# Kernel tuning notes

Measured on AMD Instinct MI355X. Metric: run time of the kernel, lower is better.

The kernel has to match this reference:

```python
import jax, jax.numpy as jnp
import numpy as np
import math

D_MODEL = 128
N_HEADS = 8
D_FF = 512
FACTOR = 3
EPS = 1e-5


def _ln(x, g, b):
    mu = x.mean(-1, keepdims=True)
    var = ((x - mu) ** 2).mean(-1, keepdims=True)
    return (x - mu) / jnp.sqrt(var + EPS) * g + b


def setup_inputs() -> dict:
    key = jax.random.key(0)
    ks = jax.random.split(key, 16)
    d, dff = D_MODEL, D_FF
    s = 0.02
    return {
        "x": jax.random.normal(ks[0], (4, 32, 256), dtype=jnp.float32),
        "mlp_w": jax.random.normal(ks[1], (d,)) * s,  # Conv2d(1,d,1x1) weight squeezed
        "mlp_b": jnp.zeros((d,), jnp.float32),
        "wq": jax.random.normal(ks[2], (d, d)) * s, "bq": jnp.zeros((d,), jnp.float32),
        "wk": jax.random.normal(ks[3], (d, d)) * s, "bk": jnp.zeros((d,), jnp.float32),
        "wv": jax.random.normal(ks[4], (d, d)) * s, "bv": jnp.zeros((d,), jnp.float32),
        "wo": jax.random.normal(ks[5], (d, d)) * s, "bo": jnp.zeros((d,), jnp.float32),
        "w1": jax.random.normal(ks[6], (dff, d)) * s, "b1": jnp.zeros((dff,), jnp.float32),
        "w2": jax.random.normal(ks[7], (d, dff)) * s, "b2": jnp.zeros((d,), jnp.float32),
        "ln1_g": jnp.ones((d,), jnp.float32), "ln1_b": jnp.zeros((d,), jnp.float32),
        "ln2_g": jnp.ones((d,), jnp.float32), "ln2_b": jnp.zeros((d,), jnp.float32),
    }


def reference(x, mlp_w, mlp_b, wq, bq, wk, bk, wv, bv, wo, bo,
              w1, b1, w2, b2, ln1_g, ln1_b, ln2_g, ln2_b):
    b, N, T = x.shape
    C, H = D_MODEL, N_HEADS
    E = C // H
    # 1x1 Conv2d from 1 channel -> per-channel affine of scalar input
    h = x[..., None] * mlp_w + mlp_b                      # [b,N,T,C]
    h = h.reshape(b * N, T, C)                            # [B,L,C]
    B, L = h.shape[0], T
    q = (h @ wq.T + bq).reshape(B, L, H, E).transpose(0, 2, 1, 3)  # [B,H,L,E]
    k = (h @ wk.T + bk).reshape(B, L, H, E).transpose(0, 2, 1, 3)
    v = (h @ wv.T + bv).reshape(B, L, H, E).transpose(0, 2, 1, 3)

    sample_k = min(FACTOR * math.ceil(math.log(L)), L)
    u = min(FACTOR * math.ceil(math.log(L)), L)
    # random K-sample indices shared across batch/heads (torch.randint analogue)
    idx = jax.random.randint(jax.random.key(42), (L, sample_k), 0, L)

    scores_full = jnp.einsum('bhle,bhse->bhls', q, k)     # [B,H,L,L]
    qk_sample = jnp.take_along_axis(scores_full, idx[None, None], axis=-1)  # [B,H,L,sample_k]
    M = qk_sample.max(-1) - qk_sample.sum(-1) / L         # sparsity measure
    m_top = jax.lax.top_k(M, u)[1]                        # [B,H,u] top-u query indices
    scores_top = jnp.take_along_axis(scores_full, m_top[..., None], axis=2)  # [B,H,u,L]
    scores_top = scores_top / math.sqrt(E)

    attn = jax.nn.softmax(scores_top, axis=-1)
    upd = jnp.einsum('bhul,bhle->bhue', attn, v)          # [B,H,u,E]
    # mask_flag=False: initial context = mean(V) broadcast over queries
    context = jnp.broadcast_to(v.mean(axis=2, keepdims=True), v.shape)
    bi = jnp.arange(B)[:, None, None]
    hi = jnp.arange(H)[None, :, None]
    context = context.at[bi, hi, m_top].set(upd)          # scatter top-u updates

    out = context.transpose(0, 2, 1, 3).reshape(B, L, C) @ wo.T + bo
    x1 = _ln(h + out, ln1_g, ln1_b)
    y = jax.nn.relu(x1 @ w1.T + b1) @ w2.T + b2           # 1x1 conv1d pair == MLP
    out2 = _ln(x1 + y, ln2_g, ln2_b)
    out2 = out2.reshape(b, N, T, C).sum(axis=1)           # sum over N
    return out2.transpose(0, 2, 1)                        # [b,C,T]
```

## Files before the change

kernel.cpp:

```cpp
#include <hip/hip_runtime.h>
#include <stdint.h>
#include <math.h>


#define EPSF 1e-5f

typedef short bf16x8 __attribute__((ext_vector_type(8)));
typedef float f32x4  __attribute__((ext_vector_type(4)));

__device__ __forceinline__ unsigned short f2bf(float f) {
  union { float f; unsigned u; } v; v.f = f;
  unsigned r = v.u + 0x7FFFu + ((v.u >> 16) & 1u);
  return (unsigned short)(r >> 16);
}
__device__ __forceinline__ float bf2f(unsigned short u) {
  union { unsigned u; float f; } v; v.u = ((unsigned)u) << 16;
  return v.f;
}
__device__ __forceinline__ float waveSum(float v) {
  #pragma unroll
  for (int m = 32; m > 0; m >>= 1) v += __shfl_xor(v, m);
  return v;
}

__device__ __forceinline__ void threefry2x32_k42(uint32_t& x0, uint32_t& x1) {
  const uint32_t ks0 = 0u, ks1 = 42u, ks2 = 0u ^ 42u ^ 0x1BD11BDAu;
  x0 += ks0; x1 += ks1;
#define TF_R(d) { x0 += x1; x1 = (x1 << d) | (x1 >> (32 - d)); x1 ^= x0; }
  TF_R(13) TF_R(15) TF_R(26) TF_R(6)  x0 += ks1; x1 += ks2 + 1u;
  TF_R(17) TF_R(29) TF_R(16) TF_R(24) x0 += ks2; x1 += ks0 + 2u;
  TF_R(13) TF_R(15) TF_R(26) TF_R(6)  x0 += ks0; x1 += ks1 + 3u;
  TF_R(17) TF_R(29) TF_R(16) TF_R(24) x0 += ks1; x1 += ks2 + 4u;
  TF_R(13) TF_R(15) TF_R(26) TF_R(6)  x0 += ks2; x1 += ks0 + 5u;
#undef TF_R
}

__global__ __launch_bounds__(256) void setup_kernel(
    const float* __restrict__ mlp_w, const float* __restrict__ mlp_b,
    const float* __restrict__ wq, const float* __restrict__ bq,
    const float* __restrict__ wk, const float* __restrict__ bk,
    const float* __restrict__ wv, const float* __restrict__ bv,
    const float* __restrict__ wo, const float* __restrict__ bo,
    const float* __restrict__ w1, const float* __restrict__ w2,
    int* __restrict__ idxT, float* __restrict__ cst,
    unsigned short* __restrict__ w1bf, unsigned short* __restrict__ w2bf) {
  int tid = threadIdx.x;
  {
    int gid = blockIdx.x * 256 + tid;
    int base = gid * 16;
    const float* src; unsigned short* dst; int off;
    if (base < 65536) { src = w1; dst = w1bf; off = base; }
    else              { src = w2; dst = w2bf; off = base - 65536; }
    #pragma unroll 4
    for (int k = 0; k < 16; k++) dst[off + k] = f2bf(src[off + k]);
  }
  if (blockIdx.x != 0) return;
  for (int p = tid; p < 2304; p += 256) {
    uint32_t a = (uint32_t)p, bb = (uint32_t)(p + 2304);
    threefry2x32_k42(a, bb);
    int l0 = p / 18, j0 = p - l0 * 18;
    int p2 = p + 2304;
    int l1 = p2 / 18, j1 = p2 - l1 * 18;
    idxT[j0 * 256 + l0] = (int)(a & 0xFFu);
    idxT[j1 * 256 + l1] = (int)(bb & 0xFFu);
  }
  if (tid < 128) {
    float aq = 0.f, cq_ = 0.f, ak = 0.f, ck_ = 0.f, av = 0.f, cv_ = 0.f;
    for (int c = 0; c < 128; c++) {
      float w = mlp_w[c], bb = mlp_b[c];
      float q = wq[tid * 128 + c], k = wk[tid * 128 + c], v = wv[tid * 128 + c];
      aq += q * w; cq_ += q * bb;
      ak += k * w; ck_ += k * bb;
      av += v * w; cv_ += v * bb;
    }
    cst[0   + tid] = aq;
    cst[128 + tid] = cq_ + bq[tid];
    cst[256 + tid] = ak;
    cst[384 + tid] = ck_ + bk[tid];
    cst[512 + tid] = av;
    cst[640 + tid] = cv_ + bv[tid];
  }
  __syncthreads();
  if (tid < 8) {
    float a = 0.f, b = 0.f, g = 0.f, d = 0.f;
    for (int e = 0; e < 16; e++) {
      int j = tid * 16 + e;
      float Aq = cst[j], Cq = cst[128 + j], Ak = cst[256 + j], Ck = cst[384 + j];
      a += Aq * Ak; b += Aq * Ck; g += Cq * Ak; d += Cq * Ck;
    }
    cst[768 + tid] = a; cst[776 + tid] = b; cst[784 + tid] = g; cst[792 + tid] = d;
  }
  if (tid < 128) {
    float oc = 0.f;
    for (int h = 0; h < 8; h++) {
      float s = 0.f;
      for (int e = 0; e < 16; e++) {
        float w = wo[tid * 128 + h * 16 + e];
        s  += w * cst[512 + h * 16 + e];
        oc += w * cst[640 + h * 16 + e];
      }
      cst[800 + h * 128 + tid] = s;
    }
    cst[1824 + tid] = oc + bo[tid] + mlp_b[tid];
  }
}

__global__ __launch_bounds__(256) void attn_kernel(
    const float* __restrict__ x, const int* __restrict__ idxT,
    const float* __restrict__ cst, float* __restrict__ g) {
  __shared__ float xr[256];
  __shared__ float Mb[512];
  __shared__ float selv[512];
  __shared__ float rsum[4], rmax[4], rmin[4];
  __shared__ int   items[64];
  __shared__ float witem[64];
  __shared__ int   cnt;
  int tid = threadIdx.x, lane = tid & 63, w = tid >> 6;
  int seq = blockIdx.x >> 2, hg = blockIdx.x & 3;
  if (tid == 0) cnt = 0;
  float xv = x[seq * 256 + tid];
  xr[tid] = xv;
  float s = waveSum(xv);
  float mx = xv, mn = xv;
  #pragma unroll
  for (int m = 32; m > 0; m >>= 1) {
    mx = fmaxf(mx, __shfl_xor(mx, m));
    mn = fminf(mn, __shfl_xor(mn, m));
  }
  if (lane == 0) { rsum[w] = s; rmax[w] = mx; rmin[w] = mn; }
  __syncthreads();
  float meanx = (rsum[0] + rsum[1] + rsum[2] + rsum[3]) * (1.0f / 256.0f);
  float maxx = fmaxf(fmaxf(rmax[0], rmax[1]), fmaxf(rmax[2], rmax[3]));
  float minx = fminf(fminf(rmin[0], rmin[1]), fminf(rmin[2], rmin[3]));
  int l32 = tid & 31, grp = tid >> 5;
  float xs8[8];
  #pragma unroll
  for (int k = 0; k < 8; k++) xs8[k] = xr[l32 + k * 32];
  float mx18 = -INFINITY, mn18 = INFINITY, s18 = 0.f;
  #pragma unroll 3
  for (int j = 0; j < 18; j++) {
    float xs = xr[idxT[j * 256 + tid]];
    mx18 = fmaxf(mx18, xs); mn18 = fminf(mn18, xs); s18 += xs;
  }
  int h0 = hg * 2, h1 = h0 + 1;
  float al0 = cst[768 + h0], be0 = cst[776 + h0], ga0 = cst[784 + h0], de0 = cst[792 + h0];
  float al1 = cst[768 + h1], be1 = cst[776 + h1], ga1 = cst[784 + h1], de1 = cst[792 + h1];
  float ac0 = fmaf(al0, xv, ga0), cc0 = fmaf(be0, xv, de0);
  float ac1 = fmaf(al1, xv, ga1), cc1 = fmaf(be1, xv, de1);
  float M0 = ((ac0 >= 0.f ? ac0 * mx18 : ac0 * mn18) + cc0)
           - (fmaf(ac0, s18, 18.f * cc0)) * (1.0f / 256.0f);
  float M1 = ((ac1 >= 0.f ? ac1 * mx18 : ac1 * mn18) + cc1)
           - (fmaf(ac1, s18, 18.f * cc1)) * (1.0f / 256.0f);
  Mb[tid] = M0; Mb[256 + tid] = M1;
  __syncthreads();
  int r0 = 0, r1 = 0;
  const float4* Mb4 = (const float4*)Mb;
  #pragma unroll 4
  for (int j4 = 0; j4 < 64; j4++) {
    float4 a = Mb4[j4], bb = Mb4[64 + j4];
    int base = j4 * 4;
    r0 += (a.x > M0) || (a.x == M0 && base     < tid);
    r0 += (a.y > M0) || (a.y == M0 && base + 1 < tid);
    r0 += (a.z > M0) || (a.z == M0 && base + 2 < tid);
    r0 += (a.w > M0) || (a.w == M0 && base + 3 < tid);
    r1 += (bb.x > M1) || (bb.x == M1 && base     < tid);
    r1 += (bb.y > M1) || (bb.y == M1 && base + 1 < tid);
    r1 += (bb.z > M1) || (bb.z == M1 && base + 2 < tid);
    r1 += (bb.w > M1) || (bb.w == M1 && base + 3 < tid);
  }
  selv[tid] = meanx; selv[256 + tid] = meanx;
  if (r0 < 18) { int p = atomicAdd(&cnt, 1); items[p] = tid;       witem[p] = 0.25f * ac0; }
  if (r1 < 18) { int p = atomicAdd(&cnt, 1); items[p] = 256 + tid; witem[p] = 0.25f * ac1; }
  __syncthreads();
  int nIt = cnt;
  for (int i = grp; i < nIt; i += 8) {
    int it = items[i]; float wv = witem[i];
    float m0 = (wv >= 0.f) ? wv * maxx : wv * minx;
    float S1 = 0.f, Sx = 0.f;
    #pragma unroll
    for (int k = 0; k < 8; k++) {
      float e = __expf(fmaf(wv, xs8[k], -m0));
      S1 += e; Sx = fmaf(xs8[k], e, Sx);
    }
    #pragma unroll
    for (int m = 16; m > 0; m >>= 1) {
      S1 += __shfl_xor(S1, m); Sx += __shfl_xor(Sx, m);
    }
    if (l32 == 0) selv[it] = Sx / S1;
  }
  __syncthreads();
  float2 gv; gv.x = selv[tid]; gv.y = selv[256 + tid];
  *(float2*)&g[(size_t)((seq << 8) + tid) * 8 + hg * 2] = gv;
}

__global__ __launch_bounds__(256, 4) void mega_kernel(
    const float* __restrict__ x, const float* __restrict__ g,
    const float* __restrict__ cst, const float* __restrict__ mlp_w,
    const unsigned short* __restrict__ w1bf, const float* __restrict__ b1,
    const unsigned short* __restrict__ w2bf, const float* __restrict__ b2,
    const float* __restrict__ ln1g, const float* __restrict__ ln1b,
    const float* __restrict__ ln2g, const float* __restrict__ ln2b,
    float* __restrict__ out) {
  __shared__ unsigned short x1s[32 * 136];
  __shared__ char ovl[32 * 264 * 2];
  __shared__ float psum[512];
  unsigned short* a1s = (unsigned short*)ovl;
  float*          zbuf = (float*)ovl;
  int tid = threadIdx.x, lane = tid & 63, w = tid >> 6;
  int col = lane & 15, quad = lane >> 4;
  int b = blockIdx.x >> 8, t = blockIdx.x & 255;

  {
    int c0 = lane << 1;
    float mwa = mlp_w[c0], mwb = mlp_w[c0 | 1];
    float cca = cst[1824 + c0], ccb = cst[1824 + (c0 | 1)];
    float wva[8], wvb[8];
    #pragma unroll
    for (int h = 0; h < 8; h++) {
      wva[h] = cst[800 + h * 128 + c0];
      wvb[h] = cst[800 + h * 128 + (c0 | 1)];
    }
    float g1a = ln1g[c0], g1b = ln1g[c0 | 1];
    float e1a = ln1b[c0], e1b = ln1b[c0 | 1];
    for (int tk = 0; tk < 8; tk++) {
      int n = w * 8 + tk;
      int tok = ((b * 32 + n) << 8) + t;
      float xvv = x[tok];
      float4 gA = *(const float4*)(g + (size_t)tok * 8);
      float4 gB = *(const float4*)(g + (size_t)tok * 8 + 4);
      float ra = fmaf(xvv, mwa, cca), rb = fmaf(xvv, mwb, ccb);
      ra = fmaf(gA.x, wva[0], ra); rb = fmaf(gA.x, wvb[0], rb);
      ra = fmaf(gA.y, wva[1], ra); rb = fmaf(gA.y, wvb[1], rb);
      ra = fmaf(gA.z, wva[2], ra); rb = fmaf(gA.z, wvb[2], rb);
      ra = fmaf(gA.w, wva[3], ra); rb = fmaf(gA.w, wvb[3], rb);
      ra = fmaf(gB.x, wva[4], ra); rb = fmaf(gB.x, wvb[4], rb);
      ra = fmaf(gB.y, wva[5], ra); rb = fmaf(gB.y, wvb[5], rb);
      ra = fmaf(gB.z, wva[6], ra); rb = fmaf(gB.z, wvb[6], rb);
      ra = fmaf(gB.w, wva[7], ra); rb = fmaf(gB.w, wvb[7], rb);
      float su = waveSum(ra + rb);
      float mu = su * (1.0f / 128.0f);
      float da = ra - mu, db = rb - mu;
      float vs = waveSum(da * da + db * db);
      float inv = rsqrtf(vs * (1.0f / 128.0f) + EPSF);
      unsigned int pa = f2bf(da * inv * g1a + e1a);
      unsigned int pb = f2bf(db * inv * g1b + e1b);
      *(unsigned int*)&x1s[n * 136 + c0] = pa | (pb << 16);
    }
  }
  __syncthreads();

  f32x4 acc2[4];
  #pragma unroll
  for (int i = 0; i < 4; i++) acc2[i] = (f32x4){0.f, 0.f, 0.f, 0.f};

  for (int fh = 0; fh < 2; fh++) {
    f32x4 acc1[8];
    #pragma unroll
    for (int i = 0; i < 8; i++) acc1[i] = (f32x4){0.f, 0.f, 0.f, 0.f};
    #pragma unroll
    for (int ks = 0; ks < 4; ks++) {
      bf16x8 af[2];
      #pragma unroll
      for (int rg = 0; rg < 2; rg++)
        af[rg] = *(const bf16x8*)&x1s[(rg * 16 + col) * 136 + ks * 32 + quad * 8];
      #pragma unroll
      for (int ft = 0; ft < 4; ft++) {
        int f = fh * 256 + w * 64 + ft * 16 + col;
        bf16x8 bfr = *(const bf16x8*)(w1bf + f * 128 + ks * 32 + quad * 8);
        #pragma unroll
        for (int rg = 0; rg < 2; rg++)
          acc1[rg * 4 + ft] = __builtin_amdgcn_mfma_f32_16x16x32_bf16(
              af[rg], bfr, acc1[rg * 4 + ft], 0, 0, 0);
      }
    }
    if (fh) __syncthreads();
    #pragma unroll
    for (int ft = 0; ft < 4; ft++) {
      int fl = w * 64 + ft * 16 + col;
      float bv = b1[fh * 256 + fl];
      #pragma unroll
      for (int rg = 0; rg < 2; rg++) {
        f32x4 a = acc1[rg * 4 + ft];
        #pragma unroll
        for (int r = 0; r < 4; r++) {
          float vv = fmaxf(a[r] + bv, 0.f);
          a1s[(rg * 16 + quad * 4 + r) * 264 + fl] = f2bf(vv);
        }
      }
    }
    __syncthreads();
    #pragma unroll
    for (int ks = 0; ks < 8; ks++) {
      bf16x8 a2[2];
      #pragma unroll
      for (int rg = 0; rg < 2; rg++)
        a2[rg] = *(const bf16x8*)&a1s[(rg * 16 + col) * 264 + ks * 32 + quad * 8];
      #pragma unroll
      for (int tc = 0; tc < 2; tc++) {
        int c = w * 32 + tc * 16 + col;
        bf16x8 bfr = *(const bf16x8*)(w2bf + c * 512 + fh * 256 + ks * 32 + quad * 8);
        #pragma unroll
        for (int rg = 0; rg < 2; rg++)
          acc2[rg * 2 + tc] = __builtin_amdgcn_mfma_f32_16x16x32_bf16(
              a2[rg], bfr, acc2[rg * 2 + tc], 0, 0, 0);
      }
    }
  }
  __syncthreads();

  #pragma unroll
  for (int tc = 0; tc < 2; tc++) {
    int c = w * 32 + tc * 16 + col;
    float b2c = b2[c];
    #pragma unroll
    for (int rg = 0; rg < 2; rg++) {
      #pragma unroll
      for (int r = 0; r < 4; r++) {
        int row = rg * 16 + quad * 4 + r;
        float z = acc2[rg * 2 + tc][r] + b2c + bf2f(x1s[row * 136 + c]);
        zbuf[row * 132 + c] = z;
      }
    }
  }
  __syncthreads();

  {
    int rloc = lane & 7, part = lane >> 3;
    int row = w * 8 + rloc;
    float4 zv[4];
    #pragma unroll
    for (int q = 0; q < 4; q++)
      zv[q] = *(const float4*)&zbuf[row * 132 + part * 16 + q * 4];
    float s = 0.f;
    #pragma unroll
    for (int q = 0; q < 4; q++) s += zv[q].x + zv[q].y + zv[q].z + zv[q].w;
    s += __shfl_xor(s, 8); s += __shfl_xor(s, 16); s += __shfl_xor(s, 32);
    float mu = s * (1.0f / 128.0f);
    float ss = 0.f;
    #pragma unroll
    for (int q = 0; q < 4; q++) {
      float d0 = zv[q].x - mu, d1 = zv[q].y - mu, d2 = zv[q].z - mu, d3 = zv[q].w - mu;
      ss += d0 * d0 + d1 * d1 + d2 * d2 + d3 * d3;
    }
    ss += __shfl_xor(ss, 8); ss += __shfl_xor(ss, 16); ss += __shfl_xor(ss, 32);
    float inv = rsqrtf(ss * (1.0f / 128.0f) + EPSF);
    float4 o[4];
    #pragma unroll
    for (int q = 0; q < 4; q++) {
      float4 g2v = *(const float4*)(ln2g + part * 16 + q * 4);
      float4 e2v = *(const float4*)(ln2b + part * 16 + q * 4);
      o[q].x = (zv[q].x - mu) * inv * g2v.x + e2v.x;
      o[q].y = (zv[q].y - mu) * inv * g2v.y + e2v.y;
      o[q].z = (zv[q].z - mu) * inv * g2v.z + e2v.z;
      o[q].w = (zv[q].w - mu) * inv * g2v.w + e2v.w;
    }
    #pragma unroll
    for (int m = 1; m <= 4; m <<= 1) {
      #pragma unroll
      for (int q = 0; q < 4; q++) {
        o[q].x += __shfl_xor(o[q].x, m);
        o[q].y += __shfl_xor(o[q].y, m);
        o[q].z += __shfl_xor(o[q].z, m);
        o[q].w += __shfl_xor(o[q].w, m);
      }
    }
    if (rloc == 0) {
      #pragma unroll
      for (int q = 0; q < 4; q++)
        *(float4*)&psum[w * 128 + part * 16 + q * 4] = o[q];
    }
  }
  __syncthreads();
  if (tid < 128) {
    int c = tid;
    float v = psum[c] + psum[128 + c] + psum[256 + c] + psum[384 + c];
    out[(size_t)(b * 128 + c) * 256 + t] = v;
  }
}

extern "C" void kernel_launch(void* const* d_in, const int* in_sizes, int n_in,
                              void* d_out, int out_size, void* d_ws, size_t ws_size,
                              hipStream_t stream) {
  (void)in_sizes; (void)n_in; (void)out_size; (void)ws_size;
  const float* x    = (const float*)d_in[0];
  const float* mlpw = (const float*)d_in[1];
  const float* mlpb = (const float*)d_in[2];
  const float* wq   = (const float*)d_in[3];
  const float* bq   = (const float*)d_in[4];
  const float* wk   = (const float*)d_in[5];
  const float* bk   = (const float*)d_in[6];
  const float* wv   = (const float*)d_in[7];
  const float* bv   = (const float*)d_in[8];
  const float* wo   = (const float*)d_in[9];
  const float* bo   = (const float*)d_in[10];
  const float* w1   = (const float*)d_in[11];
  const float* b1   = (const float*)d_in[12];
  const float* w2   = (const float*)d_in[13];
  const float* b2   = (const float*)d_in[14];
  const float* ln1g = (const float*)d_in[15];
  const float* ln1b = (const float*)d_in[16];
  const float* ln2g = (const float*)d_in[17];
  const float* ln2b = (const float*)d_in[18];

  char* ws = (char*)d_ws;
  int*            idxT = (int*)(ws);
  float*          cst  = (float*)(ws + 20480);
  unsigned short* w1bf = (unsigned short*)(ws + 32768);
  unsigned short* w2bf = (unsigned short*)(ws + 163840);
  float*          gbuf = (float*)(ws + 294912);
  float*          outp = (float*)d_out;

  hipLaunchKernelGGL(setup_kernel, dim3(32), dim3(256), 0, stream,
                     mlpw, mlpb, wq, bq, wk, bk, wv, bv, wo, bo, w1, w2,
                     idxT, cst, w1bf, w2bf);
  hipLaunchKernelGGL(attn_kernel, dim3(512), dim3(256), 0, stream,
                     x, idxT, cst, gbuf);
  hipLaunchKernelGGL(mega_kernel, dim3(1024), dim3(256), 0, stream,
                     x, gbuf, cst, mlpw, w1bf, b1, w2bf, b2,
                     ln1g, ln1b, ln2g, ln2b, outp);
}
```

Measured before the change: 163.7 us.

## Split FFN by hidden chunks per wave, removing block barriers between GEMMs

Restructures the MLP in the fused kernel so each wave owns a 128-wide slice of the hidden dimension. It computes its partial FFN2 output over all 128 channels using a private LDS tile, so the barriers between FFN1 and FFN2 are no longer needed. The partial sums from the four waves are reduced through LDS in bf16 before LayerNorm2, which adds precision loss and extra LDS traffic. It also batches four tokens in the LN1 prologue to overlap the shuffle reductions, and lowers the launch-bounds occupancy hint from 4 to 3 to leave room for the larger accumulator set.

```diff
diff --git a/kernel.cpp b/kernel.cpp
--- a/kernel.cpp
+++ b/kernel.cpp
@@ -193,7 +193,7 @@
   *(float2*)&g[(size_t)((seq << 8) + tid) * 8 + hg * 2] = gv;
 }
 
-__global__ __launch_bounds__(256, 4) void mega_kernel(
+__global__ __launch_bounds__(256, 3) void mega_kernel(
     const float* __restrict__ x, const float* __restrict__ g,
     const float* __restrict__ cst, const float* __restrict__ mlp_w,
     const unsigned short* __restrict__ w1bf, const float* __restrict__ b1,
@@ -202,13 +202,12 @@
     const float* __restrict__ ln2g, const float* __restrict__ ln2b,
     float* __restrict__ out) {
   __shared__ unsigned short x1s[32 * 136];
-  __shared__ char ovl[32 * 264 * 2];
+  __shared__ unsigned short tbuf[4 * 2304];
   __shared__ float psum[512];
-  unsigned short* a1s = (unsigned short*)ovl;
-  float*          zbuf = (float*)ovl;
   int tid = threadIdx.x, lane = tid & 63, w = tid >> 6;
   int col = lane & 15, quad = lane >> 4;
   int b = blockIdx.x >> 8, t = blockIdx.x & 255;
+  unsigned short* tb = tbuf + w * 2304;
 
   {
     int c0 = lane << 1;
@@ -222,159 +221,194 @@
     }
     float g1a = ln1g[c0], g1b = ln1g[c0 | 1];
     float e1a = ln1b[c0], e1b = ln1b[c0 | 1];
-    for (int tk = 0; tk < 8; tk++) {
-      int n = w * 8 + tk;
-      int tok = ((b * 32 + n) << 8) + t;
-      float xvv = x[tok];
-      float4 gA = *(const float4*)(g + (size_t)tok * 8);
-      float4 gB = *(const float4*)(g + (size_t)tok * 8 + 4);
-      float ra = fmaf(xvv, mwa, cca), rb = fmaf(xvv, mwb, ccb);
-      ra = fmaf(gA.x, wva[0], ra); rb = fmaf(gA.x, wvb[0], rb);
-      ra = fmaf(gA.y, wva[1], ra); rb = fmaf(gA.y, wvb[1], rb);
-      ra = fmaf(gA.z, wva[2], ra); rb = fmaf(gA.z, wvb[2], rb);
-      ra = fmaf(gA.w, wva[3], ra); rb = fmaf(gA.w, wvb[3], rb);
-      ra = fmaf(gB.x, wva[4], ra); rb = fmaf(gB.x, wvb[4], rb);
-      ra = fmaf(gB.y, wva[5], ra); rb = fmaf(gB.y, wvb[5], rb);
-      ra = fmaf(gB.z, wva[6], ra); rb = fmaf(gB.z, wvb[6], rb);
-      ra = fmaf(gB.w, wva[7], ra); rb = fmaf(gB.w, wvb[7], rb);
-      float su = waveSum(ra + rb);
-      float mu = su * (1.0f / 128.0f);
-      float da = ra - mu, db = rb - mu;
-      float vs = waveSum(da * da + db * db);
-      float inv = rsqrtf(vs * (1.0f / 128.0f) + EPSF);
-      unsigned int pa = f2bf(da * inv * g1a + e1a);
-      unsigned int pb = f2bf(db * inv * g1b + e1b);
-      *(unsigned int*)&x1s[n * 136 + c0] = pa | (pb << 16);
-    }
-  }
-  __syncthreads();
-
-  f32x4 acc2[4];
-  #pragma unroll
-  for (int i = 0; i < 4; i++) acc2[i] = (f32x4){0.f, 0.f, 0.f, 0.f};
-
-  for (int fh = 0; fh < 2; fh++) {
-    f32x4 acc1[8];
-    #pragma unroll
-    for (int i = 0; i < 8; i++) acc1[i] = (f32x4){0.f, 0.f, 0.f, 0.f};
+    #pragma unroll
+    for (int bt = 0; bt < 2; bt++) {
+      float xv4[4]; float4 gA[4], gB[4];
+      #pragma unroll
+      for (int k = 0; k < 4; k++) {
+        int n = w * 8 + bt * 4 + k;
+        int tok = ((b * 32 + n) << 8) + t;
+        xv4[k] = x[tok];
+        gA[k] = *(const float4*)(g + (size_t)tok * 8);
+        gB[k] = *(const float4*)(g + (size_t)tok * 8 + 4);
+      }
+      float ra[4], rb[4], su[4];
+      #pragma unroll
+      for (int k = 0; k < 4; k++) {
+        float a_ = fmaf(xv4[k], mwa, cca), b_ = fmaf(xv4[k], mwb, ccb);
+        a_ = fmaf(gA[k].x, wva[0], a_); b_ = fmaf(gA[k].x, wvb[0], b_);
+        a_ = fmaf(gA[k].y, wva[1], a_); b_ = fmaf(gA[k].y, wvb[1], b_);
+        a_ = fmaf(gA[k].z, wva[2], a_); b_ = fmaf(gA[k].z, wvb[2], b_);
+        a_ = fmaf(gA[k].w, wva[3], a_); b_ = fmaf(gA[k].w, wvb[3], b_);
+        a_ = fmaf(gB[k].x, wva[4], a_); b_ = fmaf(gB[k].x, wvb[4], b_);
+        a_ = fmaf(gB[k].y, wva[5], a_); b_ = fmaf(gB[k].y, wvb[5], b_);
+        a_ = fmaf(gB[k].z, wva[6], a_); b_ = fmaf(gB[k].z, wvb[6], b_);
+        a_ = fmaf(gB[k].w, wva[7], a_); b_ = fmaf(gB[k].w, wvb[7], b_);
+        ra[k] = a_; rb[k] = b_; su[k] = a_ + b_;
+      }
+      #pragma unroll
+      for (int m = 32; m > 0; m >>= 1) {
+        su[0] += __shfl_xor(su[0], m); su[1] += __shfl_xor(su[1], m);
+        su[2] += __shfl_xor(su[2], m); su[3] += __shfl_xor(su[3], m);
+      }
+      float vs[4], da[4], db[4];
+      #pragma unroll
+      for (int k = 0; k < 4; k++) {
+        float mu = su[k] * (1.0f / 128.0f);
+        da[k] = ra[k] - mu; db[k] = rb[k] - mu;
+        vs[k] = da[k] * da[k] + db[k] * db[k];
+      }
+      #pragma unroll
+      for (int m = 32; m > 0; m >>= 1) {
+        vs[0] += __shfl_xor(vs[0], m); vs[1] += __shfl_xor(vs[1], m);
+        vs[2] += __shfl_xor(vs[2], m); vs[3] += __shfl_xor(vs[3], m);
+      }
+      #pragma unroll
+      for (int k = 0; k < 4; k++) {
+        int n = w * 8 + bt * 4 + k;
+        float inv = rsqrtf(vs[k] * (1.0f / 128.0f) + EPSF);
+        unsigned int pa = f2bf(da[k] * inv * g1a + e1a);
+        unsigned int pb = f2bf(db[k] * inv * g1b + e1b);
+        *(unsigned int*)&x1s[n * 136 + c0] = pa | (pb << 16);
+      }
+    }
+  }
+  __syncthreads();
+
+  float b1v[2][4];
+  #pragma unroll
+  for (int ch = 0; ch < 2; ch++)
+    #pragma unroll
+    for (int ft = 0; ft < 4; ft++)
+      b1v[ch][ft] = b1[w * 128 + ch * 64 + ft * 16 + col];
+
+  f32x4 acc2[2][8];
+  #pragma unroll
+  for (int i = 0; i < 2; i++)
+    #pragma unroll
+    for (int j = 0; j < 8; j++) acc2[i][j] = (f32x4){0.f, 0.f, 0.f, 0.f};
+
+  #pragma unroll
+  for (int ch = 0; ch < 2; ch++) {
+    int fbase = w * 128 + ch * 64;
+    f32x4 acc1[2][4];
+    #pragma unroll
+    for (int i = 0; i < 2; i++)
+      #pragma unroll
+      for (int j = 0; j < 4; j++) acc1[i][j] = (f32x4){0.f, 0.f, 0.f, 0.f};
     #pragma unroll
     for (int ks = 0; ks < 4; ks++) {
-      bf16x8 af[2];
-      #pragma unroll
-      for (int rg = 0; rg < 2; rg++)
-        af[rg] = *(const bf16x8*)&x1s[(rg * 16 + col) * 136 + ks * 32 + quad * 8];
+      bf16x8 a0 = *(const bf16x8*)&x1s[col * 136 + ks * 32 + quad * 8];
+      bf16x8 a1 = *(const bf16x8*)&x1s[(16 + col) * 136 + ks * 32 + quad * 8];
       #pragma unroll
       for (int ft = 0; ft < 4; ft++) {
-        int f = fh * 256 + w * 64 + ft * 16 + col;
-        bf16x8 bfr = *(const bf16x8*)(w1bf + f * 128 + ks * 32 + quad * 8);
-        #pragma unroll
-        for (int rg = 0; rg < 2; rg++)
-          acc1[rg * 4 + ft] = __builtin_amdgcn_mfma_f32_16x16x32_bf16(
-              af[rg], bfr, acc1[rg * 4 + ft], 0, 0, 0);
-      }
-    }
-    if (fh) __syncthreads();
+        int f = fbase + ft * 16 + col;
+        bf16x8 bw = *(const bf16x8*)(w1bf + f * 128 + ks * 32 + quad * 8);
+        acc1[0][ft] = __builtin_amdgcn_mfma_f32_16x16x32_bf16(a0, bw, acc1[0][ft], 0, 0, 0);
+        acc1[1][ft] = __builtin_amdgcn_mfma_f32_16x16x32_bf16(a1, bw, acc1[1][ft], 0, 0, 0);
+      }
+    }
     #pragma unroll
     for (int ft = 0; ft < 4; ft++) {
-      int fl = w * 64 + ft * 16 + col;
-      float bv = b1[fh * 256 + fl];
       #pragma unroll
       for (int rg = 0; rg < 2; rg++) {
-        f32x4 a = acc1[rg * 4 + ft];
         #pragma unroll
         for (int r = 0; r < 4; r++) {
-          float vv = fmaxf(a[r] + bv, 0.f);
-          a1s[(rg * 16 + quad * 4 + r) * 264 + fl] = f2bf(vv);
+          float vv = fmaxf(acc1[rg][ft][r] + b1v[ch][ft], 0.f);
+          tb[(rg * 16 + quad * 4 + r) * 72 + ft * 16 + col] = f2bf(vv);
         }
       }
     }
+    #pragma unroll
+    for (int kk = 0; kk < 2; kk++) {
+      bf16x8 a0 = *(const bf16x8*)&tb[col * 72 + kk * 32 + quad * 8];
+      bf16x8 a1 = *(const bf16x8*)&tb[(16 + col) * 72 + kk * 32 + quad * 8];
+      int kg = fbase + kk * 32 + quad * 8;
+      #pragma unroll
+      for (int tc = 0; tc < 8; tc++) {
+        int c = tc * 16 + col;
+        bf16x8 bw = *(const bf16x8*)(w2bf + c * 512 + kg);
+        acc2[0][tc] = __builtin_amdgcn_mfma_f32_16x16x32_bf16(a0, bw, acc2[0][tc], 0, 0, 0);
+        acc2[1][tc] = __builtin_amdgcn_mfma_f32_16x16x32_bf16(a1, bw, acc2[1][tc], 0, 0, 0);
+      }
+    }
+  }
+
+  int row16 = tid >> 4, c8 = (tid & 15) << 3;
+  float b2v[8], g2v[8], e2v[8];
+  {
+    float4 a0 = *(const float4*)(b2 + c8),  a1 = *(const float4*)(b2 + c8 + 4);
+    float4 b0 = *(const float4*)(ln2g + c8), b1_ = *(const float4*)(ln2g + c8 + 4);
+    float4 c0 = *(const float4*)(ln2b + c8), c1 = *(const float4*)(ln2b + c8 + 4);
+    b2v[0]=a0.x; b2v[1]=a0.y; b2v[2]=a0.z; b2v[3]=a0.w;
+    b2v[4]=a1.x; b2v[5]=a1.y; b2v[6]=a1.z; b2v[7]=a1.w;
+    g2v[0]=b0.x; g2v[1]=b0.y; g2v[2]=b0.z; g2v[3]=b0.w;
+    g2v[4]=b1_.x; g2v[5]=b1_.y; g2v[6]=b1_.z; g2v[7]=b1_.w;
+    e2v[0]=c0.x; e2v[1]=c0.y; e2v[2]=c0.z; e2v[3]=c0.w;
+    e2v[4]=c1.x; e2v[5]=c1.y; e2v[6]=c1.z; e2v[7]=c1.w;
+  }
+  float res[2][8];
+  #pragma unroll
+  for (int p = 0; p < 2; p++) {
+    bf16x8 rv = *(const bf16x8*)&x1s[(p * 16 + row16) * 136 + c8];
+    #pragma unroll
+    for (int k = 0; k < 8; k++) res[p][k] = bf2f((unsigned short)rv[k]);
+  }
+
+  #pragma unroll
+  for (int p = 0; p < 2; p++) {
+    if (p) __syncthreads();
+    #pragma unroll
+    for (int tc = 0; tc < 8; tc++) {
+      #pragma unroll
+      for (int r = 0; r < 4; r++)
+        tb[(quad * 4 + r) * 136 + tc * 16 + col] = f2bf(acc2[p][tc][r]);
+    }
     __syncthreads();
-    #pragma unroll
-    for (int ks = 0; ks < 8; ks++) {
-      bf16x8 a2[2];
-      #pragma unroll
-      for (int rg = 0; rg < 2; rg++)
-        a2[rg] = *(const bf16x8*)&a1s[(rg * 16 + col) * 264 + ks * 32 + quad * 8];
-      #pragma unroll
-      for (int tc = 0; tc < 2; tc++) {
-        int c = w * 32 + tc * 16 + col;
-        bf16x8 bfr = *(const bf16x8*)(w2bf + c * 512 + fh * 256 + ks * 32 + quad * 8);
+    float z[8];
+    #pragma unroll
+    for (int k = 0; k < 8; k++) z[k] = b2v[k] + res[p][k];
+    #pragma unroll
+    for (int ws = 0; ws < 4; ws++) {
+      bf16x8 v = *(const bf16x8*)&tbuf[ws * 2304 + row16 * 136 + c8];
+      #pragma unroll
+      for (int k = 0; k < 8; k++) z[k] += bf2f((unsigned short)v[k]);
+    }
+    float s = 0.f;
+    #pragma unroll
+    for (int k = 0; k < 8; k++) s += z[k];
+    #pragma unroll
+    for (int m = 1; m <= 8; m <<= 1) s += __shfl_xor(s, m);
+    float mu = s * (1.0f / 128.0f);
+    float q = 0.f;
+    #pragma unroll
+    for (int k = 0; k < 8; k++) { float d = z[k] - mu; q += d * d; }
+    #pragma unroll
+    for (int m = 1; m <= 8; m <<= 1) q += __shfl_xor(q, m);
+    float inv = rsqrtf(q * (1.0f / 128.0f) + EPSF);
+    float o[8];
+    #pragma unroll
+    for (int k = 0; k < 8; k++) o[k] = (z[k] - mu) * inv * g2v[k] + e2v[k];
+    #pragma unroll
+    for (int k = 0; k < 8; k++) {
+      o[k] += __shfl_xor(o[k], 16);
+      o[k] += __shfl_xor(o[k], 32);
+    }
+    if (lane < 16) {
+      float* pp = &psum[w * 128 + lane * 8];
+      if (p == 0) {
         #pragma unroll
-        for (int rg = 0; rg < 2; rg++)
-          acc2[rg * 2 + tc] = __builtin_amdgcn_mfma_f32_16x16x32_bf16(
-              a2[rg], bfr, acc2[rg * 2 + tc], 0, 0, 0);
-      }
-    }
-  }
-  __syncthreads();
-
-  #pragma unroll
-  for (int tc = 0; tc < 2; tc++) {
-    int c = w * 32 + tc * 16 + col;
-    float b2c = b2[c];
-    #pragma unroll
-    for (int rg = 0; rg < 2; rg++) {
-      #pragma unroll
-      for (int r = 0; r < 4; r++) {
-        int row = rg * 16 + quad * 4 + r;
-        float z = acc2[rg * 2 + tc][r] + b2c + bf2f(x1s[row * 136 + c]);
-        zbuf[row * 132 + c] = z;
-      }
-    }
-  }
-  __syncthreads();
-
-  {
-    int rloc = lane & 7, part = lane >> 3;
-    int row = w * 8 + rloc;
-    float4 zv[4];
-    #pragma unroll
-    for (int q = 0; q < 4; q++)
-      zv[q] = *(const float4*)&zbuf[row * 132 + part * 16 + q * 4];
-    float s = 0.f;
-    #pragma unroll
-    for (int q = 0; q < 4; q++) s += zv[q].x + zv[q].y + zv[q].z + zv[q].w;
-    s += __shfl_xor(s, 8); s += __shfl_xor(s, 16); s += __shfl_xor(s, 32);
-    float mu = s * (1.0f / 128.0f);
-    float ss = 0.f;
-    #pragma unroll
-    for (int q = 0; q < 4; q++) {
-      float d0 = zv[q].x - mu, d1 = zv[q].y - mu, d2 = zv[q].z - mu, d3 = zv[q].w - mu;
-      ss += d0 * d0 + d1 * d1 + d2 * d2 + d3 * d3;
-    }
-    ss += __shfl_xor(ss, 8); ss += __shfl_xor(ss, 16); ss += __shfl_xor(ss, 32);
-    float inv = rsqrtf(ss * (1.0f / 128.0f) + EPSF);
-    float4 o[4];
-    #pragma unroll
-    for (int q = 0; q < 4; q++) {
-      float4 g2v = *(const float4*)(ln2g + part * 16 + q * 4);
-      float4 e2v = *(const float4*)(ln2b + part * 16 + q * 4);
-      o[q].x = (zv[q].x - mu) * inv * g2v.x + e2v.x;
-      o[q].y = (zv[q].y - mu) * inv * g2v.y + e2v.y;
-      o[q].z = (zv[q].z - mu) * inv * g2v.z + e2v.z;
-      o[q].w = (zv[q].w - mu) * inv * g2v.w + e2v.w;
-    }
-    #pragma unroll
-    for (int m = 1; m <= 4; m <<= 1) {
-      #pragma unroll
-      for (int q = 0; q < 4; q++) {
-        o[q].x += __shfl_xor(o[q].x, m);
-        o[q].y += __shfl_xor(o[q].y, m);
-        o[q].z += __shfl_xor(o[q].z, m);
-        o[q].w += __shfl_xor(o[q].w, m);
-      }
-    }
-    if (rloc == 0) {
-      #pragma unroll
-      for (int q = 0; q < 4; q++)
-        *(float4*)&psum[w * 128 + part * 16 + q * 4] = o[q];
+        for (int k = 0; k < 8; k++) pp[k] = o[k];
+      } else {
+        #pragma unroll
+        for (int k = 0; k < 8; k++) pp[k] += o[k];
+      }
     }
   }
   __syncthreads();
   if (tid < 128) {
-    int c = tid;
-    float v = psum[c] + psum[128 + c] + psum[256 + c] + psum[384 + c];
-    out[(size_t)(b * 128 + c) * 256 + t] = v;
+    float v = psum[tid] + psum[128 + tid] + psum[256 + tid] + psum[384 + tid];
+    out[(size_t)(b * 128 + tid) * 256 + t] = v;
   }
 }
 
```

Result: slower. 170.0 us (+3.8%).
